# Kernel optimization log

Measured on AMD Instinct MI355X. Metric: run time of the kernel, lower is better.

## Reference

```python
import jax, jax.numpy as jnp
import numpy as np

E, H, O = 64, 128, 16  # enc_hidden_dim, dec_hidden_dim, dec_output_dim (proj_size)
B, N, FUT = 64, 1000, 12


def _lstm_proj_cell(x, h, c, W_ih, W_hh, b_ih, b_hh, W_hr):
    # PyTorch gate order: input, forget, cell(g), output
    gates = x @ W_ih.T + h @ W_hh.T + (b_ih + b_hh)
    i, f, g, o = jnp.split(gates, 4, axis=-1)
    c_new = jax.nn.sigmoid(f) * c + jax.nn.sigmoid(i) * jnp.tanh(g)
    h_full = jax.nn.sigmoid(o) * jnp.tanh(c_new)
    h_new = h_full @ W_hr.T  # proj_size projection
    return h_new, c_new


def setup_inputs() -> dict:
    key = jax.random.key(0)
    ks = jax.random.split(key, 20)
    sc = 0.1
    inp = {
        "enc_outputs": jax.random.normal(ks[0], (B, 1, N, E), jnp.float32),
        "mean": jax.random.normal(ks[1], (B, FUT, N, O), jnp.float32),
        "s": jax.random.normal(ks[2], (1, O), jnp.float32),
        "h_0": jax.random.normal(ks[3], (2, O), jnp.float32),
        "c_0": jax.random.normal(ks[4], (2, H), jnp.float32),
        "W_ih_l0": sc * jax.random.normal(ks[5], (4 * H, E + O), jnp.float32),
        "W_hh_l0": sc * jax.random.normal(ks[6], (4 * H, O), jnp.float32),
        "b_ih_l0": sc * jax.random.normal(ks[7], (4 * H,), jnp.float32),
        "b_hh_l0": sc * jax.random.normal(ks[8], (4 * H,), jnp.float32),
        "W_hr_l0": sc * jax.random.normal(ks[9], (O, H), jnp.float32),
        "W_ih_l1": sc * jax.random.normal(ks[10], (4 * H, O), jnp.float32),
        "W_hh_l1": sc * jax.random.normal(ks[11], (4 * H, O), jnp.float32),
        "b_ih_l1": sc * jax.random.normal(ks[12], (4 * H,), jnp.float32),
        "b_hh_l1": sc * jax.random.normal(ks[13], (4 * H,), jnp.float32),
        "W_hr_l1": sc * jax.random.normal(ks[14], (O, H), jnp.float32),
        "future": FUT,
    }
    # forget-gate bias = 1.0 as in reset_bias()
    for nme in ("b_ih_l0", "b_hh_l0", "b_ih_l1", "b_hh_l1"):
        inp[nme] = inp[nme].at[H:2 * H].set(1.0)
    return inp


def _forward(enc_outputs, mean, s, h_0, c_0,
             W_ih_l0, W_hh_l0, b_ih_l0, b_hh_l0, W_hr_l0,
             W_ih_l1, W_hh_l1, b_ih_l1, b_hh_l1, W_hr_l1, future):
    b, _, n_nodes, _ = enc_outputs.shape
    enc = enc_outputs[:, 0]            # [B, N, E]
    node_mean = jnp.mean(mean, axis=1)  # [B, N, O]
    # state is carried across nodes AND timesteps: one chain of N*future steps
    node_idx = jnp.arange(n_nodes * future) // future

    last0 = jnp.broadcast_to(s[0], (b, s.shape[1]))
    h1_0 = jnp.broadcast_to(h_0[0], (b, h_0.shape[1]))
    h2_0 = jnp.broadcast_to(h_0[1], (b, h_0.shape[1]))
    c1_0 = jnp.broadcast_to(c_0[0], (b, c_0.shape[1]))
    c2_0 = jnp.broadcast_to(c_0[1], (b, c_0.shape[1]))

    def step(carry, n):
        last, h1, c1, h2, c2 = carry
        enc_t = jnp.take(enc, n, axis=1)        # [B, E]
        nm_t = jnp.take(node_mean, n, axis=1)   # [B, O]
        loop = last + nm_t                      # TFRate forced to 0.0 in source
        x = jnp.concatenate([enc_t, loop], axis=-1)
        h1, c1 = _lstm_proj_cell(x, h1, c1, W_ih_l0, W_hh_l0, b_ih_l0, b_hh_l0, W_hr_l0)
        h2, c2 = _lstm_proj_cell(h1, h2, c2, W_ih_l1, W_hh_l1, b_ih_l1, b_hh_l1, W_hr_l1)
        return (h2, h1, c1, h2, c2), h2 + nm_t

    _, outs = jax.lax.scan(step, (last0, h1_0, c1_0, h2_0, c2_0), node_idx)
    # outs: [N*future, B, O] -> [B, future, N, O]
    outs = outs.reshape(n_nodes, future, b, -1).transpose(2, 1, 0, 3)
    return outs


def reference(enc_outputs, mean, s, h_0, c_0,
              W_ih_l0, W_hh_l0, b_ih_l0, b_hh_l0, W_hr_l0,
              W_ih_l1, W_hh_l1, b_ih_l1, b_hh_l1, W_hr_l1, future):
    return _forward(enc_outputs, mean, s, h_0, c_0,
                    W_ih_l0, W_hh_l0, b_ih_l0, b_hh_l0, W_hr_l0,
                    W_ih_l1, W_hh_l1, b_ih_l1, b_hh_l1, W_hr_l1, future)
```

## Files before the change

### kernel.cpp

```cpp
#include <hip/hip_runtime.h>

#define BB 64
#define NN 1000
#define FF 12
#define EE 64
#define HH 128
#define OO 16
#define GG 512

__device__ __forceinline__ float rcp_(float x){ return __builtin_amdgcn_rcpf(x); }
__device__ __forceinline__ float sigm_(float x){ return rcp_(1.0f + __expf(-x)); }
__device__ __forceinline__ float tanh_(float x){ return 1.0f - 2.0f*rcp_(__expf(2.0f*x) + 1.0f); }

__global__ __launch_bounds__(512, 2)
void decoder_kernel(const float* __restrict__ enc,
                    const float* __restrict__ mean,
                    const float* __restrict__ sv,
                    const float* __restrict__ h0,
                    const float* __restrict__ c0,
                    const float* __restrict__ Wih0,
                    const float* __restrict__ Whh0,
                    const float* __restrict__ bih0,
                    const float* __restrict__ bhh0,
                    const float* __restrict__ Whr0,
                    const float* __restrict__ Wih1,
                    const float* __restrict__ Whh1,
                    const float* __restrict__ bih1,
                    const float* __restrict__ bhh1,
                    const float* __restrict__ Whr1,
                    float* __restrict__ out)
{
    const int t = threadIdx.x;
    const int b = blockIdx.x;

    __shared__ float s_last[OO];
    __shared__ float s_h1[OO];
    __shared__ float s_h2[OO];
    __shared__ float s_gates[GG];
    __shared__ float s_hfull[HH];
    __shared__ float s_enc[EE];
    __shared__ float s_nm[OO];

    float w_enc[EE];
    float w_loop[OO], w_hh0[OO], w_ih1[OO], w_hh1[OO];
    {
        const float* r = Wih0 + t*(EE+OO);
        #pragma unroll
        for (int e=0;e<EE;e++) w_enc[e] = r[e];
        #pragma unroll
        for (int j=0;j<OO;j++) w_loop[j] = r[EE+j];
        #pragma unroll
        for (int j=0;j<OO;j++) w_hh0[j] = Whh0[t*OO+j];
        #pragma unroll
        for (int j=0;j<OO;j++) w_ih1[j] = Wih1[t*OO+j];
        #pragma unroll
        for (int j=0;j<OO;j++) w_hh1[j] = Whh1[t*OO+j];
    }
    const float bias0 = bih0[t] + bhh0[t];
    const float bias1 = bih1[t] + bhh1[t];

    const int j16 = t >> 5;
    const int kb  = (t & 31) * 4;
    float wp0[4], wp1[4];
    #pragma unroll
    for (int u=0;u<4;u++){
        wp0[u] = Whr0[j16*HH + kb + u];
        wp1[u] = Whr1[j16*HH + kb + u];
    }

    float c1 = (t < HH) ? c0[t]      : 0.0f;
    float c2 = (t < HH) ? c0[HH + t] : 0.0f;
    if (t < OO){
        s_last[t] = sv[t];
        s_h1[t]   = h0[t];
        s_h2[t]   = h0[OO + t];
    }
    __syncthreads();

    const float* encB  = enc  + (size_t)b * NN * EE;
    const float* meanB = mean + (size_t)b * FF * NN * OO;
    float*       outB  = out  + (size_t)b * FF * NN * OO;

    const bool isTanhGate = ((t >> 7) == 2);

    for (int n = 0; n < NN; ++n){
        if (t < EE){
            s_enc[t] = encB[n*EE + t];
        } else if (t < EE + OO){
            const int j = t - EE;
            float a = 0.0f;
            #pragma unroll
            for (int f=0; f<FF; ++f) a += meanB[(f*NN + n)*OO + j];
            s_nm[j] = a * (1.0f/12.0f);
        }
        __syncthreads();

        float pre0 = bias0;
        #pragma unroll
        for (int e=0;e<EE;e++) pre0 += s_enc[e]*w_enc[e];
        #pragma unroll
        for (int j=0;j<OO;j++) pre0 += s_nm[j]*w_loop[j];

        for (int f=0; f<FF; ++f){
            float acc = pre0;
            #pragma unroll
            for (int j=0;j<OO;j++) acc += s_last[j]*w_loop[j];
            #pragma unroll
            for (int j=0;j<OO;j++) acc += s_h1[j]*w_hh0[j];
            s_gates[t] = isTanhGate ? tanh_(acc) : sigm_(acc);
            __syncthreads();

            if (t < HH){
                float iv = s_gates[t],      fv = s_gates[HH + t];
                float gv = s_gates[2*HH+t], ov = s_gates[3*HH + t];
                c1 = fv*c1 + iv*gv;
                s_hfull[t] = ov * tanh_(c1);
            }
            __syncthreads();

            {
                float p = s_hfull[kb+0]*wp0[0] + s_hfull[kb+1]*wp0[1]
                        + s_hfull[kb+2]*wp0[2] + s_hfull[kb+3]*wp0[3];
                p += __shfl_down(p, 16, 32);
                p += __shfl_down(p,  8, 32);
                p += __shfl_down(p,  4, 32);
                p += __shfl_down(p,  2, 32);
                p += __shfl_down(p,  1, 32);
                if ((t & 31) == 0) s_h1[j16] = p;
            }
            __syncthreads();

            float acc1 = bias1;
            #pragma unroll
            for (int j=0;j<OO;j++) acc1 += s_h1[j]*w_ih1[j];
            #pragma unroll
            for (int j=0;j<OO;j++) acc1 += s_h2[j]*w_hh1[j];
            s_gates[t] = isTanhGate ? tanh_(acc1) : sigm_(acc1);
            __syncthreads();

            if (t < HH){
                float iv = s_gates[t],      fv = s_gates[HH + t];
                float gv = s_gates[2*HH+t], ov = s_gates[3*HH + t];
                c2 = fv*c2 + iv*gv;
                s_hfull[t] = ov * tanh_(c2);
            }
            __syncthreads();

            {
                float p = s_hfull[kb+0]*wp1[0] + s_hfull[kb+1]*wp1[1]
                        + s_hfull[kb+2]*wp1[2] + s_hfull[kb+3]*wp1[3];
                p += __shfl_down(p, 16, 32);
                p += __shfl_down(p,  8, 32);
                p += __shfl_down(p,  4, 32);
                p += __shfl_down(p,  2, 32);
                p += __shfl_down(p,  1, 32);
                if ((t & 31) == 0){
                    s_h2[j16]   = p;
                    s_last[j16] = p;
                    outB[(f*NN + n)*OO + j16] = p + s_nm[j16];
                }
            }
            __syncthreads();
        }
    }
}

extern "C" void kernel_launch(void* const* d_in, const int* in_sizes, int n_in,
                              void* d_out, int out_size, void* d_ws, size_t ws_size,
                              hipStream_t stream) {
    const float* enc  = (const float*)d_in[0];
    const float* mean = (const float*)d_in[1];
    const float* sv   = (const float*)d_in[2];
    const float* h0   = (const float*)d_in[3];
    const float* c0   = (const float*)d_in[4];
    const float* Wih0 = (const float*)d_in[5];
    const float* Whh0 = (const float*)d_in[6];
    const float* bih0 = (const float*)d_in[7];
    const float* bhh0 = (const float*)d_in[8];
    const float* Whr0 = (const float*)d_in[9];
    const float* Wih1 = (const float*)d_in[10];
    const float* Whh1 = (const float*)d_in[11];
    const float* bih1 = (const float*)d_in[12];
    const float* bhh1 = (const float*)d_in[13];
    const float* Whr1 = (const float*)d_in[14];
    float* out = (float*)d_out;

    decoder_kernel<<<dim3(BB), dim3(512), 0, stream>>>(
        enc, mean, sv, h0, c0,
        Wih0, Whh0, bih0, bhh0, Whr0,
        Wih1, Whh1, bih1, bhh1, Whr1,
        out);
}
```

Measured before the change: 15.59 ms.

## Fuse LSTM cell update into projection reduction, removing a barrier per layer

The cell-state update and hidden output are now computed redundantly by every 32-lane group for its 4 hidden units, then fed straight into the projection reduction. This removes the s_hfull stage and one __syncthreads per layer per timestep. Cell state lives in double-buffered shared arrays so the redundant readers never race the writer. Launch bounds are relaxed to one block per CU, giving more registers. The cost is 16x redundant gate reads and tanh work per step.

```diff
diff --git a/kernel.cpp b/kernel.cpp
--- a/kernel.cpp
+++ b/kernel.cpp
@@ -12,7 +12,7 @@
 __device__ __forceinline__ float sigm_(float x){ return rcp_(1.0f + __expf(-x)); }
 __device__ __forceinline__ float tanh_(float x){ return 1.0f - 2.0f*rcp_(__expf(2.0f*x) + 1.0f); }
 
-__global__ __launch_bounds__(512, 2)
+__global__ __launch_bounds__(512, 1)
 void decoder_kernel(const float* __restrict__ enc,
                     const float* __restrict__ mean,
                     const float* __restrict__ sv,
@@ -33,13 +33,14 @@
     const int t = threadIdx.x;
     const int b = blockIdx.x;
 
-    __shared__ float s_last[OO];
-    __shared__ float s_h1[OO];
-    __shared__ float s_h2[OO];
-    __shared__ float s_gates[GG];
-    __shared__ float s_hfull[HH];
-    __shared__ float s_enc[EE];
-    __shared__ float s_nm[OO];
+    __shared__ __align__(16) float s_gates[GG];
+    __shared__ __align__(16) float s_c1[2][HH];
+    __shared__ __align__(16) float s_c2[2][HH];
+    __shared__ __align__(16) float s_h1[OO];
+    __shared__ __align__(16) float s_h2[OO];
+    __shared__ __align__(16) float s_last[OO];
+    __shared__ __align__(16) float s_enc[EE];
+    __shared__ __align__(16) float s_nm[OO];
 
     float w_enc[EE];
     float w_loop[OO], w_hh0[OO], w_ih1[OO], w_hh1[OO];
@@ -59,8 +60,9 @@
     const float bias0 = bih0[t] + bhh0[t];
     const float bias1 = bih1[t] + bhh1[t];
 
-    const int j16 = t >> 5;
-    const int kb  = (t & 31) * 4;
+    const int j16  = t >> 5;
+    const int lane = t & 31;
+    const int kb   = lane * 4;
     float wp0[4], wp1[4];
     #pragma unroll
     for (int u=0;u<4;u++){
@@ -68,12 +70,17 @@
         wp1[u] = Whr1[j16*HH + kb + u];
     }
 
-    float c1 = (t < HH) ? c0[t]      : 0.0f;
-    float c2 = (t < HH) ? c0[HH + t] : 0.0f;
     if (t < OO){
         s_last[t] = sv[t];
         s_h1[t]   = h0[t];
         s_h2[t]   = h0[OO + t];
+    }
+    if (t < 32){
+        #pragma unroll
+        for (int u=0;u<4;u++){
+            s_c1[0][t*4+u] = c0[t*4+u];
+            s_c2[0][t*4+u] = c0[HH + t*4+u];
+        }
     }
     __syncthreads();
 
@@ -100,6 +107,9 @@
         for (int e=0;e<EE;e++) pre0 += s_enc[e]*w_enc[e];
         #pragma unroll
         for (int j=0;j<OO;j++) pre0 += s_nm[j]*w_loop[j];
+        const float nm_j = s_nm[j16];
+
+        int par = 0;
 
         for (int f=0; f<FF; ++f){
             float acc = pre0;
@@ -110,23 +120,27 @@
             s_gates[t] = isTanhGate ? tanh_(acc) : sigm_(acc);
             __syncthreads();
 
-            if (t < HH){
-                float iv = s_gates[t],      fv = s_gates[HH + t];
-                float gv = s_gates[2*HH+t], ov = s_gates[3*HH + t];
-                c1 = fv*c1 + iv*gv;
-                s_hfull[t] = ov * tanh_(c1);
-            }
-            __syncthreads();
-
             {
-                float p = s_hfull[kb+0]*wp0[0] + s_hfull[kb+1]*wp0[1]
-                        + s_hfull[kb+2]*wp0[2] + s_hfull[kb+3]*wp0[3];
+                const float4 gi = *reinterpret_cast<const float4*>(&s_gates[kb]);
+                const float4 gf = *reinterpret_cast<const float4*>(&s_gates[HH + kb]);
+                const float4 gg = *reinterpret_cast<const float4*>(&s_gates[2*HH + kb]);
+                const float4 go = *reinterpret_cast<const float4*>(&s_gates[3*HH + kb]);
+                float4 cv = *reinterpret_cast<const float4*>(&s_c1[par][kb]);
+                cv.x = gf.x*cv.x + gi.x*gg.x;
+                cv.y = gf.y*cv.y + gi.y*gg.y;
+                cv.z = gf.z*cv.z + gi.z*gg.z;
+                cv.w = gf.w*cv.w + gi.w*gg.w;
+                float p = go.x*tanh_(cv.x)*wp0[0]
+                        + go.y*tanh_(cv.y)*wp0[1]
+                        + go.z*tanh_(cv.z)*wp0[2]
+                        + go.w*tanh_(cv.w)*wp0[3];
                 p += __shfl_down(p, 16, 32);
                 p += __shfl_down(p,  8, 32);
                 p += __shfl_down(p,  4, 32);
                 p += __shfl_down(p,  2, 32);
                 p += __shfl_down(p,  1, 32);
-                if ((t & 31) == 0) s_h1[j16] = p;
+                if (lane == 0) s_h1[j16] = p;
+                if (t < 32) *reinterpret_cast<float4*>(&s_c1[par^1][t*4]) = cv;
             }
             __syncthreads();
 
@@ -138,29 +152,35 @@
             s_gates[t] = isTanhGate ? tanh_(acc1) : sigm_(acc1);
             __syncthreads();
 
-            if (t < HH){
-                float iv = s_gates[t],      fv = s_gates[HH + t];
-                float gv = s_gates[2*HH+t], ov = s_gates[3*HH + t];
-                c2 = fv*c2 + iv*gv;
-                s_hfull[t] = ov * tanh_(c2);
-            }
-            __syncthreads();
-
             {
-                float p = s_hfull[kb+0]*wp1[0] + s_hfull[kb+1]*wp1[1]
-                        + s_hfull[kb+2]*wp1[2] + s_hfull[kb+3]*wp1[3];
+                const float4 gi = *reinterpret_cast<const float4*>(&s_gates[kb]);
+                const float4 gf = *reinterpret_cast<const float4*>(&s_gates[HH + kb]);
+                const float4 gg = *reinterpret_cast<const float4*>(&s_gates[2*HH + kb]);
+                const float4 go = *reinterpret_cast<const float4*>(&s_gates[3*HH + kb]);
+                float4 cv = *reinterpret_cast<const float4*>(&s_c2[par][kb]);
+                cv.x = gf.x*cv.x + gi.x*gg.x;
+                cv.y = gf.y*cv.y + gi.y*gg.y;
+                cv.z = gf.z*cv.z + gi.z*gg.z;
+                cv.w = gf.w*cv.w + gi.w*gg.w;
+                float p = go.x*tanh_(cv.x)*wp1[0]
+                        + go.y*tanh_(cv.y)*wp1[1]
+                        + go.z*tanh_(cv.z)*wp1[2]
+                        + go.w*tanh_(cv.w)*wp1[3];
                 p += __shfl_down(p, 16, 32);
                 p += __shfl_down(p,  8, 32);
                 p += __shfl_down(p,  4, 32);
                 p += __shfl_down(p,  2, 32);
                 p += __shfl_down(p,  1, 32);
-                if ((t & 31) == 0){
+                if (lane == 0){
                     s_h2[j16]   = p;
                     s_last[j16] = p;
-                    outB[(f*NN + n)*OO + j16] = p + s_nm[j16];
+                    outB[(f*NN + n)*OO + j16] = p + nm_j;
                 }
+                if (t < 32) *reinterpret_cast<float4*>(&s_c2[par^1][t*4]) = cv;
             }
             __syncthreads();
+
+            par ^= 1;
         }
     }
 }
```

Result: slower. 17.83 ms (+14.4%).

## Halve block to 256 threads, pair gates per thread with shuffle exchange, prefetch inputs

Applied to the files above, without the earlier changes.

Each thread now computes two gate rows, (i,g) or (f,o), and exchanges partial results with its neighbour lane through a shuffle. This fuses the gate nonlinearity and the cell update into one phase and drops one barrier per LSTM cell, so each step has four barriers instead of six. The next node's encoder row and mean values are prefetched into registers so global loads overlap compute, and the projection uses float4 shared reads over 16 lanes. In exchange, register pressure roughly doubles per thread, and occupancy is limited to 256 threads per block.

```diff
diff --git a/kernel.cpp b/kernel.cpp
--- a/kernel.cpp
+++ b/kernel.cpp
@@ -6,13 +6,12 @@
 #define EE 64
 #define HH 128
 #define OO 16
-#define GG 512
 
 __device__ __forceinline__ float rcp_(float x){ return __builtin_amdgcn_rcpf(x); }
 __device__ __forceinline__ float sigm_(float x){ return rcp_(1.0f + __expf(-x)); }
 __device__ __forceinline__ float tanh_(float x){ return 1.0f - 2.0f*rcp_(__expf(2.0f*x) + 1.0f); }
 
-__global__ __launch_bounds__(512, 2)
+__global__ __launch_bounds__(256, 1)
 void decoder_kernel(const float* __restrict__ enc,
                     const float* __restrict__ mean,
                     const float* __restrict__ sv,
@@ -33,131 +32,166 @@
     const int t = threadIdx.x;
     const int b = blockIdx.x;
 
-    __shared__ float s_last[OO];
-    __shared__ float s_h1[OO];
-    __shared__ float s_h2[OO];
-    __shared__ float s_gates[GG];
-    __shared__ float s_hfull[HH];
-    __shared__ float s_enc[EE];
-    __shared__ float s_nm[OO];
-
-    float w_enc[EE];
-    float w_loop[OO], w_hh0[OO], w_ih1[OO], w_hh1[OO];
+    const int u  = t >> 1;
+    const int m  = t & 1;
+    const int rA = m*HH + u;
+    const int rB = m*HH + 2*HH + u;
+
+    const int j16 = t >> 4;
+    const int kq  = t & 15;
+    const int kc  = kq * 8;
+
+    __shared__ __align__(16) float s_hfull[HH];
+    __shared__ __align__(16) float s_h1[OO];
+    __shared__ __align__(16) float s_h2[OO];
+    __shared__ __align__(16) float s_last[OO];
+    __shared__ __align__(16) float s_enc[EE];
+    __shared__ __align__(16) float s_nm[OO];
+
+    float wAe[EE], wBe[EE];
+    float wAl[OO], wBl[OO];
+    float wAh[OO], wBh[OO];
+    float w1Ai[OO], w1Bi[OO];
+    float w1Ah[OO], w1Bh[OO];
     {
-        const float* r = Wih0 + t*(EE+OO);
-        #pragma unroll
-        for (int e=0;e<EE;e++) w_enc[e] = r[e];
-        #pragma unroll
-        for (int j=0;j<OO;j++) w_loop[j] = r[EE+j];
-        #pragma unroll
-        for (int j=0;j<OO;j++) w_hh0[j] = Whh0[t*OO+j];
-        #pragma unroll
-        for (int j=0;j<OO;j++) w_ih1[j] = Wih1[t*OO+j];
-        #pragma unroll
-        for (int j=0;j<OO;j++) w_hh1[j] = Whh1[t*OO+j];
-    }
-    const float bias0 = bih0[t] + bhh0[t];
-    const float bias1 = bih1[t] + bhh1[t];
-
-    const int j16 = t >> 5;
-    const int kb  = (t & 31) * 4;
-    float wp0[4], wp1[4];
+        const float* ra = Wih0 + (size_t)rA*(EE+OO);
+        const float* rb = Wih0 + (size_t)rB*(EE+OO);
+        #pragma unroll
+        for (int e=0;e<EE;e++){ wAe[e]=ra[e]; wBe[e]=rb[e]; }
+        #pragma unroll
+        for (int j=0;j<OO;j++){ wAl[j]=ra[EE+j]; wBl[j]=rb[EE+j]; }
+        #pragma unroll
+        for (int j=0;j<OO;j++){ wAh[j]=Whh0[rA*OO+j]; wBh[j]=Whh0[rB*OO+j]; }
+        #pragma unroll
+        for (int j=0;j<OO;j++){ w1Ai[j]=Wih1[rA*OO+j]; w1Bi[j]=Wih1[rB*OO+j]; }
+        #pragma unroll
+        for (int j=0;j<OO;j++){ w1Ah[j]=Whh1[rA*OO+j]; w1Bh[j]=Whh1[rB*OO+j]; }
+    }
+    const float b0A = bih0[rA] + bhh0[rA];
+    const float b0B = bih0[rB] + bhh0[rB];
+    const float b1A = bih1[rA] + bhh1[rA];
+    const float b1B = bih1[rB] + bhh1[rB];
+
+    float wp0[8], wp1[8];
     #pragma unroll
-    for (int u=0;u<4;u++){
-        wp0[u] = Whr0[j16*HH + kb + u];
-        wp1[u] = Whr1[j16*HH + kb + u];
-    }
-
-    float c1 = (t < HH) ? c0[t]      : 0.0f;
-    float c2 = (t < HH) ? c0[HH + t] : 0.0f;
+    for (int k=0;k<8;k++){
+        wp0[k] = Whr0[j16*HH + kc + k];
+        wp1[k] = Whr1[j16*HH + kc + k];
+    }
+
+    float c1u = c0[u];
+    float c2u = c0[HH + u];
+
     if (t < OO){
         s_last[t] = sv[t];
         s_h1[t]   = h0[t];
         s_h2[t]   = h0[OO + t];
     }
-    __syncthreads();
 
     const float* encB  = enc  + (size_t)b * NN * EE;
     const float* meanB = mean + (size_t)b * FF * NN * OO;
     float*       outB  = out  + (size_t)b * FF * NN * OO;
 
-    const bool isTanhGate = ((t >> 7) == 2);
+    float4 pf_enc = make_float4(0.f,0.f,0.f,0.f);
+    float  pf_nm[FF];
+    if (t < 16){
+        pf_enc = ((const float4*)encB)[t];
+    } else if (t < 32){
+        const int j = t - 16;
+        #pragma unroll
+        for (int ff=0; ff<FF; ++ff) pf_nm[ff] = meanB[(ff*NN + 0)*OO + j];
+    }
+    __syncthreads();
 
     for (int n = 0; n < NN; ++n){
-        if (t < EE){
-            s_enc[t] = encB[n*EE + t];
-        } else if (t < EE + OO){
-            const int j = t - EE;
+        if (t < 16){
+            ((float4*)s_enc)[t] = pf_enc;
+        } else if (t < 32){
             float a = 0.0f;
             #pragma unroll
-            for (int f=0; f<FF; ++f) a += meanB[(f*NN + n)*OO + j];
-            s_nm[j] = a * (1.0f/12.0f);
+            for (int ff=0; ff<FF; ++ff) a += pf_nm[ff];
+            s_nm[t-16] = a * (1.0f/12.0f);
         }
         __syncthreads();
 
-        float pre0 = bias0;
-        #pragma unroll
-        for (int e=0;e<EE;e++) pre0 += s_enc[e]*w_enc[e];
-        #pragma unroll
-        for (int j=0;j<OO;j++) pre0 += s_nm[j]*w_loop[j];
-
-        for (int f=0; f<FF; ++f){
-            float acc = pre0;
+        const int n1 = (n+1 < NN) ? (n+1) : n;
+        if (t < 16){
+            pf_enc = ((const float4*)encB)[n1*16 + t];
+        } else if (t < 32){
+            const int j = t - 16;
             #pragma unroll
-            for (int j=0;j<OO;j++) acc += s_last[j]*w_loop[j];
-            #pragma unroll
-            for (int j=0;j<OO;j++) acc += s_h1[j]*w_hh0[j];
-            s_gates[t] = isTanhGate ? tanh_(acc) : sigm_(acc);
-            __syncthreads();
-
-            if (t < HH){
-                float iv = s_gates[t],      fv = s_gates[HH + t];
-                float gv = s_gates[2*HH+t], ov = s_gates[3*HH + t];
-                c1 = fv*c1 + iv*gv;
-                s_hfull[t] = ov * tanh_(c1);
-            }
-            __syncthreads();
-
-            {
-                float p = s_hfull[kb+0]*wp0[0] + s_hfull[kb+1]*wp0[1]
-                        + s_hfull[kb+2]*wp0[2] + s_hfull[kb+3]*wp0[3];
-                p += __shfl_down(p, 16, 32);
-                p += __shfl_down(p,  8, 32);
-                p += __shfl_down(p,  4, 32);
-                p += __shfl_down(p,  2, 32);
-                p += __shfl_down(p,  1, 32);
-                if ((t & 31) == 0) s_h1[j16] = p;
-            }
-            __syncthreads();
-
-            float acc1 = bias1;
-            #pragma unroll
-            for (int j=0;j<OO;j++) acc1 += s_h1[j]*w_ih1[j];
-            #pragma unroll
-            for (int j=0;j<OO;j++) acc1 += s_h2[j]*w_hh1[j];
-            s_gates[t] = isTanhGate ? tanh_(acc1) : sigm_(acc1);
-            __syncthreads();
-
-            if (t < HH){
-                float iv = s_gates[t],      fv = s_gates[HH + t];
-                float gv = s_gates[2*HH+t], ov = s_gates[3*HH + t];
-                c2 = fv*c2 + iv*gv;
-                s_hfull[t] = ov * tanh_(c2);
-            }
-            __syncthreads();
-
-            {
-                float p = s_hfull[kb+0]*wp1[0] + s_hfull[kb+1]*wp1[1]
-                        + s_hfull[kb+2]*wp1[2] + s_hfull[kb+3]*wp1[3];
-                p += __shfl_down(p, 16, 32);
-                p += __shfl_down(p,  8, 32);
-                p += __shfl_down(p,  4, 32);
-                p += __shfl_down(p,  2, 32);
-                p += __shfl_down(p,  1, 32);
-                if ((t & 31) == 0){
+            for (int ff=0; ff<FF; ++ff) pf_nm[ff] = meanB[(ff*NN + n1)*OO + j];
+        }
+
+        float preA = b0A, preB = b0B;
+        #pragma unroll
+        for (int e=0;e<EE;e++){ const float ev = s_enc[e]; preA += ev*wAe[e]; preB += ev*wBe[e]; }
+        #pragma unroll
+        for (int j=0;j<OO;j++){ const float nv = s_nm[j]; preA += nv*wAl[j]; preB += nv*wBl[j]; }
+        const float nmj = s_nm[j16];
+
+        #pragma unroll 1
+        for (int f = 0; f < FF; ++f){
+            {
+                float aA = preA, aB = preB;
+                #pragma unroll
+                for (int j=0;j<OO;j++){ const float lv = s_last[j]; aA += lv*wAl[j]; aB += lv*wBl[j]; }
+                #pragma unroll
+                for (int j=0;j<OO;j++){ const float hv = s_h1[j];   aA += hv*wAh[j]; aB += hv*wBh[j]; }
+                const float gA = sigm_(aA);
+                const float gB = (m==0) ? tanh_(aB) : sigm_(aB);
+                const float sendv = (m==0) ? gA*gB : gA;
+                const float recvv = __shfl_xor(sendv, 1, 64);
+                const float Fv   = (m==0) ? recvv : sendv;
+                const float prod = (m==0) ? sendv : recvv;
+                c1u = Fv*c1u + prod;
+                if (m==1) s_hfull[u] = gB * tanh_(c1u);
+            }
+            __syncthreads();
+
+            {
+                const float4 ha = *(const float4*)&s_hfull[kc];
+                const float4 hb = *(const float4*)&s_hfull[kc+4];
+                float p = ha.x*wp0[0] + ha.y*wp0[1] + ha.z*wp0[2] + ha.w*wp0[3]
+                        + hb.x*wp0[4] + hb.y*wp0[5] + hb.z*wp0[6] + hb.w*wp0[7];
+                p += __shfl_xor(p, 8, 64);
+                p += __shfl_xor(p, 4, 64);
+                p += __shfl_xor(p, 2, 64);
+                p += __shfl_xor(p, 1, 64);
+                if (kq == 0) s_h1[j16] = p;
+            }
+            __syncthreads();
+
+            {
+                float aA = b1A, aB = b1B;
+                #pragma unroll
+                for (int j=0;j<OO;j++){ const float hv = s_h1[j]; aA += hv*w1Ai[j]; aB += hv*w1Bi[j]; }
+                #pragma unroll
+                for (int j=0;j<OO;j++){ const float hv = s_h2[j]; aA += hv*w1Ah[j]; aB += hv*w1Bh[j]; }
+                const float gA = sigm_(aA);
+                const float gB = (m==0) ? tanh_(aB) : sigm_(aB);
+                const float sendv = (m==0) ? gA*gB : gA;
+                const float recvv = __shfl_xor(sendv, 1, 64);
+                const float Fv   = (m==0) ? recvv : sendv;
+                const float prod = (m==0) ? sendv : recvv;
+                c2u = Fv*c2u + prod;
+                if (m==1) s_hfull[u] = gB * tanh_(c2u);
+            }
+            __syncthreads();
+
+            {
+                const float4 ha = *(const float4*)&s_hfull[kc];
+                const float4 hb = *(const float4*)&s_hfull[kc+4];
+                float p = ha.x*wp1[0] + ha.y*wp1[1] + ha.z*wp1[2] + ha.w*wp1[3]
+                        + hb.x*wp1[4] + hb.y*wp1[5] + hb.z*wp1[6] + hb.w*wp1[7];
+                p += __shfl_xor(p, 8, 64);
+                p += __shfl_xor(p, 4, 64);
+                p += __shfl_xor(p, 2, 64);
+                p += __shfl_xor(p, 1, 64);
+                if (kq == 0){
                     s_h2[j16]   = p;
                     s_last[j16] = p;
-                    outB[(f*NN + n)*OO + j16] = p + s_nm[j16];
+                    outB[(f*NN + n)*OO + j16] = p + nmj;
                 }
             }
             __syncthreads();
@@ -185,7 +219,7 @@
     const float* Whr1 = (const float*)d_in[14];
     float* out = (float*)d_out;
 
-    decoder_kernel<<<dim3(BB), dim3(512), 0, stream>>>(
+    decoder_kernel<<<dim3(BB), dim3(256), 0, stream>>>(
         enc, mean, sv, h0, c0,
         Wih0, Whh0, bih0, bhh0, Whr0,
         Wih1, Whh1, bih1, bhh1, Whr1,
```

After: 16.14 ms. 3.5% more time.
